# Performance work log

Measured on AMD Instinct MI355X. Metric: run time of the kernel, lower is better.

Reference implementation:

```python
import jax, jax.numpy as jnp
import numpy as np

N = 65536
IN_FEAT = 512
OUT_FEAT = 512
K = 16


def setup_inputs() -> dict:
    key = jax.random.key(0)
    k_feat, k_wt, k_wp, k_idx = jax.random.split(key, 4)
    feat = jax.random.normal(k_feat, (N, IN_FEAT), dtype=jnp.float32)
    # nn.Linear(in, out, bias=False): y = x @ W.T with W [out, in].
    # We store W as [in, out] so y = x @ W (same math, transposed layout).
    scale = 1.0 / np.sqrt(IN_FEAT)
    W_theta = jax.random.uniform(k_wt, (IN_FEAT, OUT_FEAT), dtype=jnp.float32, minval=-scale, maxval=scale)
    W_phi = jax.random.uniform(k_wp, (IN_FEAT, OUT_FEAT), dtype=jnp.float32, minval=-scale, maxval=scale)
    src_ind = jax.random.randint(k_idx, (N, K), 0, N, dtype=jnp.int64)
    return {"k": K, "src_ind": src_ind, "feat": feat, "W_theta": W_theta, "W_phi": W_phi}


def reference(k, src_ind, feat, W_theta, W_phi):
    # Dense projections (cuBLAS-friendly part)
    h_theta = feat @ W_theta            # [N, out]
    h_phi = feat @ W_phi                # [N, out]
    h_src = h_theta                     # message contribution from source node
    h_dst = h_phi - h_theta             # per-destination additive term
    # fused_edgeconv_op: result[i] = max_{j in 0..k} (h_src[src_ind[i, j]] + h_dst[i]).
    # h_dst[i] is constant over neighbors, so max commutes with the add:
    neigh = h_src[src_ind[:, :k]]       # [N, k, out] irregular gather
    result = jnp.max(neigh, axis=1) + h_dst  # [N, out]
    return result
```

## Files before the change

kernel.cpp:

```cpp
#include <hip/hip_runtime.h>
#include <hip/hip_bf16.h>
#include <stdint.h>


typedef __bf16 bf16x8 __attribute__((ext_vector_type(8)));
typedef float f32x4 __attribute__((ext_vector_type(4)));
typedef unsigned short u16x8 __attribute__((ext_vector_type(8)));

__device__ __forceinline__ unsigned short f2bf(float x) {
    unsigned u = __float_as_uint(x);
    unsigned r = u + 0x7fffu + ((u >> 16) & 1u);
    return (unsigned short)(r >> 16);
}

__device__ __forceinline__ void async_ld16(const void* g, void* l) {
    __builtin_amdgcn_global_load_lds(
        (const __attribute__((address_space(1))) unsigned int*)g,
        (__attribute__((address_space(3))) unsigned int*)l,
        16, 0, 0);
}

__global__ void k_prep_w(const float* __restrict__ Wth,
                         const float* __restrict__ Wph,
                         unsigned short* __restrict__ wtc) {
    __shared__ float tile[32][33];
    const int k0 = (blockIdx.x & 15) * 32;
    const int n0 = (blockIdx.x >> 4) * 32;
    const int t  = threadIdx.x;
    const int cc = t & 31;
    const int r0 = t >> 5;
#pragma unroll
    for (int it = 0; it < 4; ++it) {
        const int r  = it * 8 + r0;
        const int gn = n0 + cc;
        float v;
        if (gn < 512) v = Wth[(k0 + r) * 512 + gn];
        else          v = Wph[(k0 + r) * 512 + (gn - 512)] - Wth[(k0 + r) * 512 + (gn - 512)];
        tile[r][cc] = v;
    }
    __syncthreads();
#pragma unroll
    for (int it = 0; it < 4; ++it) {
        const int r2 = t & 31;
        const int c2 = it * 8 + (t >> 5);
        wtc[(size_t)(n0 + c2) * 512 + k0 + r2] = f2bf(tile[r2][c2]);
    }
}

__global__ __launch_bounds__(256, 3)
void k_gemm(const float* __restrict__ A,
            const unsigned short* __restrict__ Bt,
            unsigned short* __restrict__ theta,
            float* __restrict__ delta_f,
            size_t slabStride)
{
    __shared__ __align__(16) unsigned short As[2][128 * 32];
    __shared__ __align__(16) unsigned short Bs[2][128 * 32];

    const int tid  = threadIdx.x;
    const int wave = tid >> 6;
    const int lane = tid & 63;
    const int quad = lane >> 4;
    const int l15  = lane & 15;

    const int b  = blockIdx.x;
    const int mt = (b >> 6) * 8 + (b & 7);
    const int nt = (b >> 3) & 7;
    const int m0 = mt * 128;
    const int n0 = nt * 128;

    const int wm = wave >> 1;
    const int wn = wave & 1;

    f32x4 acc[4][4];
#pragma unroll
    for (int i = 0; i < 4; i++)
#pragma unroll
        for (int j = 0; j < 4; j++) acc[i][j] = (f32x4){0.f, 0.f, 0.f, 0.f};

    const int r0 = wave * 32 + (lane >> 2);
    const int r1 = r0 + 16;
    const int sw = (((lane & 3) ^ ((lane >> 3) & 3)) << 3);

    const float* Ag0 = A + (size_t)(m0 + r0) * 512 + (lane & 3) * 8;
    const float* Ag1 = A + (size_t)(m0 + r1) * 512 + (lane & 3) * 8;
    const unsigned short* Bg0 = Bt + (size_t)(n0 + r0) * 512 + sw;
    const unsigned short* Bg1 = Bt + (size_t)(n0 + r1) * 512 + sw;

    const int wAo0 = r0 * 32 + sw;
    const int wAo1 = r1 * 32 + sw;
    const int oB0  = wave * 1024;
    const int oB1  = wave * 1024 + 512;

    f32x4 a0lo, a0hi, a1lo, a1hi;

#define DMAB(buf, kg) do {                              \
        async_ld16(Bg0 + (kg), &Bs[(buf)][oB0]);        \
        async_ld16(Bg1 + (kg), &Bs[(buf)][oB1]);        \
    } while (0)
#define ALOAD(kg) do {                                  \
        a0lo = *(const f32x4*)(Ag0 + (kg));             \
        a0hi = *(const f32x4*)(Ag0 + (kg) + 4);         \
        a1lo = *(const f32x4*)(Ag1 + (kg));             \
        a1hi = *(const f32x4*)(Ag1 + (kg) + 4);         \
    } while (0)
#define ACVTW(buf) do {                                                       \
        u16x8 p0, p1;                                                         \
        p0[0] = f2bf(a0lo[0]); p0[1] = f2bf(a0lo[1]);                         \
        p0[2] = f2bf(a0lo[2]); p0[3] = f2bf(a0lo[3]);                         \
        p0[4] = f2bf(a0hi[0]); p0[5] = f2bf(a0hi[1]);                         \
        p0[6] = f2bf(a0hi[2]); p0[7] = f2bf(a0hi[3]);                         \
        p1[0] = f2bf(a1lo[0]); p1[1] = f2bf(a1lo[1]);                         \
        p1[2] = f2bf(a1lo[2]); p1[3] = f2bf(a1lo[3]);                         \
        p1[4] = f2bf(a1hi[0]); p1[5] = f2bf(a1hi[1]);                         \
        p1[6] = f2bf(a1hi[2]); p1[7] = f2bf(a1hi[3]);                         \
        *(u16x8*)&As[(buf)][wAo0] = p0;                                       \
        *(u16x8*)&As[(buf)][wAo1] = p1;                                       \
    } while (0)

    DMAB(0, 0);
    ALOAD(0);
    ACVTW(0);
    __syncthreads();

    const int rdoff = (quad << 3) ^ (((l15 >> 1) & 3) << 3);

#pragma unroll
    for (int kt = 0; kt < 16; ++kt) {
        const int cur = kt & 1;
        if (kt < 15) {
            DMAB(cur ^ 1, (kt + 1) * 32);
            ALOAD((kt + 1) * 32);
        }

        bf16x8 af[4], bfr[4];
#pragma unroll
        for (int t = 0; t < 4; ++t) {
            const int am = wm * 64 + t * 16 + l15;
            af[t]  = *(const bf16x8*)&As[cur][am * 32 + rdoff];
            const int bn = wn * 64 + t * 16 + l15;
            bfr[t] = *(const bf16x8*)&Bs[cur][bn * 32 + rdoff];
        }
#pragma unroll
        for (int i = 0; i < 4; i++)
#pragma unroll
            for (int j = 0; j < 4; j++)
                acc[i][j] = __builtin_amdgcn_mfma_f32_16x16x32_bf16(bfr[j], af[i], acc[i][j], 0, 0, 0);

        if (kt < 15) {
            ACVTW(cur ^ 1);
            __syncthreads();
        }
    }
#undef DMAB
#undef ALOAD
#undef ACVTW

    const bool is_theta = (n0 < 512);
#pragma unroll
    for (int i = 0; i < 4; i++) {
        const int m = m0 + wm * 64 + i * 16 + l15;
#pragma unroll
        for (int j = 0; j < 4; j++) {
            const int nb = n0 + wn * 64 + j * 16 + quad * 4;
            const f32x4 v = acc[i][j];
            if (is_theta) {
                ushort4 o;
                o.x = f2bf(v[0]); o.y = f2bf(v[1]);
                o.z = f2bf(v[2]); o.w = f2bf(v[3]);
                *(ushort4*)&theta[(size_t)(nb >> 5) * slabStride
                                  + (size_t)m * 32 + (nb & 31)] = o;
            } else {
                *(f32x4*)&delta_f[(size_t)m * 512 + (nb - 512)] = v;
            }
        }
    }
}

__global__ void k_gather(const unsigned short* __restrict__ theta,
                         float* out,
                         const int* __restrict__ src,
                         const int* __restrict__ kptr,
                         int phase, size_t slabStride)
{
    const int b     = blockIdx.x;
    const int xcd   = b & 7;
    const int chunk = b >> 3;
    const int slice = phase * 8 + xcd;
    const int kk    = *kptr;

    const unsigned short* slab = theta + (size_t)slice * slabStride;
    const int tid = threadIdx.x;
    const int c8  = (tid & 3) * 8;
    const int rly = tid >> 2;

#pragma unroll 2
    for (int pass = 0; pass < 4; ++pass) {
        const int row = chunk * 256 + pass * 64 + rly;

        float m0 = -INFINITY, m1 = -INFINITY, m2 = -INFINITY, m3 = -INFINITY;
        float m4 = -INFINITY, m5 = -INFINITY, m6 = -INFINITY, m7 = -INFINITY;

        if (kk == 16) {
            const int4* sp = (const int4*)(src + (size_t)row * 16);
            int4 sv[4];
            sv[0] = sp[0]; sv[1] = sp[1]; sv[2] = sp[2]; sv[3] = sp[3];
#pragma unroll
            for (int q = 0; q < 4; ++q) {
                const int ss[4] = {sv[q].x, sv[q].y, sv[q].z, sv[q].w};
#pragma unroll
                for (int j = 0; j < 4; ++j) {
                    const uint4 v = *(const uint4*)(slab + (size_t)ss[j] * 32 + c8);
                    m0 = fmaxf(m0, __uint_as_float(v.x << 16));
                    m1 = fmaxf(m1, __uint_as_float(v.x & 0xffff0000u));
                    m2 = fmaxf(m2, __uint_as_float(v.y << 16));
                    m3 = fmaxf(m3, __uint_as_float(v.y & 0xffff0000u));
                    m4 = fmaxf(m4, __uint_as_float(v.z << 16));
                    m5 = fmaxf(m5, __uint_as_float(v.z & 0xffff0000u));
                    m6 = fmaxf(m6, __uint_as_float(v.w << 16));
                    m7 = fmaxf(m7, __uint_as_float(v.w & 0xffff0000u));
                }
            }
        } else {
            for (int k = 0; k < kk; ++k) {
                const int s = src[(size_t)row * 16 + k];
                const uint4 v = *(const uint4*)(slab + (size_t)s * 32 + c8);
                m0 = fmaxf(m0, __uint_as_float(v.x << 16));
                m1 = fmaxf(m1, __uint_as_float(v.x & 0xffff0000u));
                m2 = fmaxf(m2, __uint_as_float(v.y << 16));
                m3 = fmaxf(m3, __uint_as_float(v.y & 0xffff0000u));
                m4 = fmaxf(m4, __uint_as_float(v.z << 16));
                m5 = fmaxf(m5, __uint_as_float(v.z & 0xffff0000u));
                m6 = fmaxf(m6, __uint_as_float(v.w << 16));
                m7 = fmaxf(m7, __uint_as_float(v.w & 0xffff0000u));
            }
        }

        float* op = out + (size_t)row * 512 + slice * 32 + c8;
        const f32x4 d0 = __builtin_nontemporal_load((const f32x4*)op);
        const f32x4 d1 = __builtin_nontemporal_load((const f32x4*)op + 1);
        f32x4 o0, o1;
        o0[0] = m0 + d0[0]; o0[1] = m1 + d0[1]; o0[2] = m2 + d0[2]; o0[3] = m3 + d0[3];
        o1[0] = m4 + d1[0]; o1[1] = m5 + d1[1]; o1[2] = m6 + d1[2]; o1[3] = m7 + d1[3];
        __builtin_nontemporal_store(o0, (f32x4*)op);
        __builtin_nontemporal_store(o1, (f32x4*)op + 1);
    }
}

extern "C" void kernel_launch(void* const* d_in, const int* in_sizes, int n_in,
                              void* d_out, int out_size, void* d_ws, size_t ws_size,
                              hipStream_t stream) {
    const int*   kptr = (const int*)d_in[0];
    const int*   src  = (const int*)d_in[1];
    const float* feat = (const float*)d_in[2];
    const float* Wth  = (const float*)d_in[3];
    const float* Wph  = (const float*)d_in[4];
    float* out = (float*)d_out;

    const int N = in_sizes[2] / 512;
    const size_t slabStride = (size_t)N * 32;

    unsigned short* wtc   = (unsigned short*)d_ws;
    unsigned short* table = (unsigned short*)((char*)d_ws + (size_t)16 * 1024 * 1024);

    k_prep_w<<<512, 256, 0, stream>>>(Wth, Wph, wtc);
    k_gemm<<<(N / 128) * 8, 256, 0, stream>>>(feat, wtc, table, out, slabStride);
    k_gather<<<8 * (N / 256), 256, 0, stream>>>(table, out, src, kptr, 0, slabStride);
    k_gather<<<8 * (N / 256), 256, 0, stream>>>(table, out, src, kptr, 1, slabStride);
}
```

Measured before the change: 493.1 us.

## Triple-buffer GEMM K-loop with explicit waitcnts and merge gather launches

The GEMM K-loop moves from double to triple LDS buffering. A-tile global loads are issued two iterations ahead through inline-asm loads, with explicit vmcnt/lgkmcnt waits and raw s_barrier replacing __syncthreads, so memory latency overlaps more MFMA work. The two gather launches are merged into one kernel in which each block processes 512 rows instead of 256, removing a launch and its tail. The cost is more LDS per block, which may reduce occupancy, more live registers, and fragile hand-written waitcnt counts.

```diff
diff --git a/kernel.cpp b/kernel.cpp
--- a/kernel.cpp
+++ b/kernel.cpp
@@ -18,6 +18,12 @@
         (const __attribute__((address_space(1))) unsigned int*)g,
         (__attribute__((address_space(3))) unsigned int*)l,
         16, 0, 0);
+}
+
+__device__ __forceinline__ f32x4 ald16(const float* p) {
+    f32x4 d;
+    asm volatile("global_load_dwordx4 %0, %1, off" : "=v"(d) : "v"(p));
+    return d;
 }
 
 __global__ void k_prep_w(const float* __restrict__ Wth,
@@ -54,8 +60,8 @@
             float* __restrict__ delta_f,
             size_t slabStride)
 {
-    __shared__ __align__(16) unsigned short As[2][128 * 32];
-    __shared__ __align__(16) unsigned short Bs[2][128 * 32];
+    __shared__ __align__(16) unsigned short As[3][128 * 32];
+    __shared__ __align__(16) unsigned short Bs[3][128 * 32];
 
     const int tid  = threadIdx.x;
     const int wave = tid >> 6;
@@ -92,45 +98,52 @@
     const int oB0  = wave * 1024;
     const int oB1  = wave * 1024 + 512;
 
-    f32x4 a0lo, a0hi, a1lo, a1hi;
+    f32x4 ar[2][4];
 
 #define DMAB(buf, kg) do {                              \
         async_ld16(Bg0 + (kg), &Bs[(buf)][oB0]);        \
         async_ld16(Bg1 + (kg), &Bs[(buf)][oB1]);        \
     } while (0)
-#define ALOAD(kg) do {                                  \
-        a0lo = *(const f32x4*)(Ag0 + (kg));             \
-        a0hi = *(const f32x4*)(Ag0 + (kg) + 4);         \
-        a1lo = *(const f32x4*)(Ag1 + (kg));             \
-        a1hi = *(const f32x4*)(Ag1 + (kg) + 4);         \
+#define ALOADQ(set, kg) do {                            \
+        ar[set][0] = ald16(Ag0 + (kg));                 \
+        ar[set][1] = ald16(Ag0 + (kg) + 4);             \
+        ar[set][2] = ald16(Ag1 + (kg));                 \
+        ar[set][3] = ald16(Ag1 + (kg) + 4);             \
     } while (0)
-#define ACVTW(buf) do {                                                       \
+#define ACVTW(set, buf) do {                                                  \
         u16x8 p0, p1;                                                         \
-        p0[0] = f2bf(a0lo[0]); p0[1] = f2bf(a0lo[1]);                         \
-        p0[2] = f2bf(a0lo[2]); p0[3] = f2bf(a0lo[3]);                         \
-        p0[4] = f2bf(a0hi[0]); p0[5] = f2bf(a0hi[1]);                         \
-        p0[6] = f2bf(a0hi[2]); p0[7] = f2bf(a0hi[3]);                         \
-        p1[0] = f2bf(a1lo[0]); p1[1] = f2bf(a1lo[1]);                         \
-        p1[2] = f2bf(a1lo[2]); p1[3] = f2bf(a1lo[3]);                         \
-        p1[4] = f2bf(a1hi[0]); p1[5] = f2bf(a1hi[1]);                         \
-        p1[6] = f2bf(a1hi[2]); p1[7] = f2bf(a1hi[3]);                         \
+        p0[0] = f2bf(ar[set][0][0]); p0[1] = f2bf(ar[set][0][1]);             \
+        p0[2] = f2bf(ar[set][0][2]); p0[3] = f2bf(ar[set][0][3]);             \
+        p0[4] = f2bf(ar[set][1][0]); p0[5] = f2bf(ar[set][1][1]);             \
+        p0[6] = f2bf(ar[set][1][2]); p0[7] = f2bf(ar[set][1][3]);             \
+        p1[0] = f2bf(ar[set][2][0]); p1[1] = f2bf(ar[set][2][1]);             \
+        p1[2] = f2bf(ar[set][2][2]); p1[3] = f2bf(ar[set][2][3]);             \
+        p1[4] = f2bf(ar[set][3][0]); p1[5] = f2bf(ar[set][3][1]);             \
+        p1[6] = f2bf(ar[set][3][2]); p1[7] = f2bf(ar[set][3][3]);             \
         *(u16x8*)&As[(buf)][wAo0] = p0;                                       \
         *(u16x8*)&As[(buf)][wAo1] = p1;                                       \
     } while (0)
 
     DMAB(0, 0);
-    ALOAD(0);
-    ACVTW(0);
-    __syncthreads();
+    ALOADQ(0, 0);
+    DMAB(1, 32);
+    ALOADQ(1, 32);
+    asm volatile("s_waitcnt vmcnt(6)" ::: "memory");
+    __builtin_amdgcn_sched_barrier(0);
+    ACVTW(0, 0);
+    asm volatile("s_waitcnt lgkmcnt(0)" ::: "memory");
+    __builtin_amdgcn_sched_barrier(0);
+    __builtin_amdgcn_s_barrier();
+    __builtin_amdgcn_sched_barrier(0);
 
     const int rdoff = (quad << 3) ^ (((l15 >> 1) & 3) << 3);
 
 #pragma unroll
     for (int kt = 0; kt < 16; ++kt) {
-        const int cur = kt & 1;
-        if (kt < 15) {
-            DMAB(cur ^ 1, (kt + 1) * 32);
-            ALOAD((kt + 1) * 32);
+        const int cur = kt % 3;
+        if (kt <= 13) {
+            DMAB((kt + 2) % 3, (kt + 2) * 32);
+            ALOADQ(kt & 1, (kt + 2) * 32);
         }
 
         bf16x8 af[4], bfr[4];
@@ -147,13 +160,19 @@
             for (int j = 0; j < 4; j++)
                 acc[i][j] = __builtin_amdgcn_mfma_f32_16x16x32_bf16(bfr[j], af[i], acc[i][j], 0, 0, 0);
 
-        if (kt < 15) {
-            ACVTW(cur ^ 1);
-            __syncthreads();
+        if (kt <= 14) {
+            if (kt <= 13) asm volatile("s_waitcnt vmcnt(6)" ::: "memory");
+            else          asm volatile("s_waitcnt vmcnt(0)" ::: "memory");
+            __builtin_amdgcn_sched_barrier(0);
+            ACVTW((kt + 1) & 1, (kt + 1) % 3);
+            asm volatile("s_waitcnt lgkmcnt(0)" ::: "memory");
+            __builtin_amdgcn_sched_barrier(0);
+            __builtin_amdgcn_s_barrier();
+            __builtin_amdgcn_sched_barrier(0);
         }
     }
 #undef DMAB
-#undef ALOAD
+#undef ALOADQ
 #undef ACVTW
 
     const bool is_theta = (n0 < 512);
@@ -181,11 +200,13 @@
                          float* out,
                          const int* __restrict__ src,
                          const int* __restrict__ kptr,
-                         int phase, size_t slabStride)
+                         int chunksPerSlice, size_t slabStride)
 {
     const int b     = blockIdx.x;
     const int xcd   = b & 7;
-    const int chunk = b >> 3;
+    const int t2    = b >> 3;
+    const int chunk = t2 % chunksPerSlice;
+    const int phase = t2 / chunksPerSlice;
     const int slice = phase * 8 + xcd;
     const int kk    = *kptr;
 
@@ -195,8 +216,8 @@
     const int rly = tid >> 2;
 
 #pragma unroll 2
-    for (int pass = 0; pass < 4; ++pass) {
-        const int row = chunk * 256 + pass * 64 + rly;
+    for (int pass = 0; pass < 8; ++pass) {
+        const int row = chunk * 512 + pass * 64 + rly;
 
         float m0 = -INFINITY, m1 = -INFINITY, m2 = -INFINITY, m3 = -INFINITY;
         float m4 = -INFINITY, m5 = -INFINITY, m6 = -INFINITY, m7 = -INFINITY;
@@ -263,8 +284,10 @@
     unsigned short* wtc   = (unsigned short*)d_ws;
     unsigned short* table = (unsigned short*)((char*)d_ws + (size_t)16 * 1024 * 1024);
 
+    const int chunksPerSlice = N / 512;
+
     k_prep_w<<<512, 256, 0, stream>>>(Wth, Wph, wtc);
     k_gemm<<<(N / 128) * 8, 256, 0, stream>>>(feat, wtc, table, out, slabStride);
-    k_gather<<<8 * (N / 256), 256, 0, stream>>>(table, out, src, kptr, 0, slabStride);
-    k_gather<<<8 * (N / 256), 256, 0, stream>>>(table, out, src, kptr, 1, slabStride);
-}
+    k_gather<<<16 * chunksPerSlice, 256, 0, stream>>>(table, out, src, kptr,
+                                                      chunksPerSlice, slabStride);
+}
```

New measurement: 514.3 us. 4.3% more time.
